# Kernel optimization log

Hardware: AMD Instinct MI355X
Metric: run time of the kernel (lower is better)

## Reference

```python
import jax, jax.numpy as jnp
import numpy as np
from jax import lax

KH = KW = 3
DIL = 4
D = DIL * (KH - 1) + 1  # dilated (effective) kernel extent = 9
PAD = 4
STRIDE = 1


def setup_inputs() -> dict:
    key = jax.random.key(0)
    k1, k2, k3, k4 = jax.random.split(key, 4)
    Cin, Cout, B, H, W = 128, 128, 16, 112, 112
    fan_in = Cin * KH * KW
    x = jax.random.normal(k1, (B, Cin, H, W), dtype=jnp.float32)
    weight = jax.random.normal(k2, (Cout, Cin, KH, KW), dtype=jnp.float32) / np.sqrt(fan_in)
    # learnable positions: offsets of each kernel point inside the dilated kernel
    P = jax.random.normal(k3, (2, Cout, Cin, KH, KW), dtype=jnp.float32) * (DIL / 2.0)
    bias = jax.random.normal(k4, (Cout,), dtype=jnp.float32) * 0.01
    return {"x": x, "weight": weight, "P": P, "bias": bias}


def _construct_kernel(weight, P):
    # Place each kernel point at its (learnable) continuous position inside the
    # D x D dilated kernel via bilinear interpolation (DCLS construction).
    O, C, kh, kw = weight.shape
    base_h = jnp.arange(kh, dtype=weight.dtype) * DIL  # regular dilated grid
    base_w = jnp.arange(kw, dtype=weight.dtype) * DIL
    p_h = jnp.clip(base_h[None, None, :, None] + P[0], 0.0, D - 1)  # (O,C,kh,kw)
    p_w = jnp.clip(base_w[None, None, None, :] + P[1], 0.0, D - 1)
    fh = jnp.floor(p_h)
    fw = jnp.floor(p_w)
    rh = p_h - fh  # fractional residuals -> bilinear weights
    rw = p_w - fw
    ih = fh.astype(jnp.int32)
    iw = fw.astype(jnp.int32)
    ih1 = jnp.minimum(ih + 1, D - 1)
    iw1 = jnp.minimum(iw + 1, D - 1)
    o = jnp.arange(O)[:, None, None, None]
    c = jnp.arange(C)[None, :, None, None]
    K = jnp.zeros((O, C, D, D), dtype=weight.dtype)
    K = K.at[o, c, ih, iw].add(weight * (1 - rh) * (1 - rw))
    K = K.at[o, c, ih1, iw].add(weight * rh * (1 - rw))
    K = K.at[o, c, ih, iw1].add(weight * (1 - rh) * rw)
    K = K.at[o, c, ih1, iw1].add(weight * rh * rw)
    return K


def reference(x, weight, P, bias):
    K = _construct_kernel(weight, P)  # (Cout, Cin, D, D)
    out = lax.conv_general_dilated(
        x, K,
        window_strides=(STRIDE, STRIDE),
        padding=[(PAD, PAD), (PAD, PAD)],
        dimension_numbers=("NCHW", "OIHW", "NCHW"),
        feature_group_count=1,
    )
    return out + bias[None, :, None, None]
```

## Files before the change

### kernel.cpp

```cpp
#include <hip/hip_runtime.h>
#include <hip/hip_bf16.h>
#include <stdint.h>


typedef __attribute__((ext_vector_type(8))) short short8;
typedef __attribute__((ext_vector_type(4))) short s16x4;
typedef __attribute__((ext_vector_type(16))) float f32x16;

__device__ inline unsigned short f2bf(float f) {
    union { float f; unsigned int u; } v; v.f = f;
    unsigned int u = v.u;
    return (unsigned short)((u + 0x7FFFu + ((u >> 16) & 1u)) >> 16);
}

__global__ void build_K(const float* __restrict__ weight,
                        const float* __restrict__ P,
                        unsigned short* __restrict__ Kws) {
    __shared__ float sacc[128 * 81];
    int tid = threadIdx.x;
    int o = blockIdx.x;
    int c = tid;
    float* a = &sacc[c * 81];
    for (int i = 0; i < 81; ++i) a[i] = 0.0f;
    int base = (o * 128 + c) * 9;
    #pragma unroll
    for (int kh = 0; kh < 3; ++kh) {
        #pragma unroll
        for (int kw = 0; kw < 3; ++kw) {
            int kk = kh * 3 + kw;
            float w  = weight[base + kk];
            float p0 = P[base + kk];
            float p1 = P[128 * 128 * 9 + base + kk];
            float ph = fminf(fmaxf((float)(kh * 4) + p0, 0.0f), 8.0f);
            float pw = fminf(fmaxf((float)(kw * 4) + p1, 0.0f), 8.0f);
            float fh = floorf(ph), fw = floorf(pw);
            float rh = ph - fh, rw = pw - fw;
            int ih = (int)fh, iw = (int)fw;
            int ih1 = min(ih + 1, 8), iw1 = min(iw + 1, 8);
            a[ih  * 9 + iw ] += w * (1.0f - rh) * (1.0f - rw);
            a[ih1 * 9 + iw ] += w * rh * (1.0f - rw);
            a[ih  * 9 + iw1] += w * (1.0f - rh) * rw;
            a[ih1 * 9 + iw1] += w * rh * rw;
        }
    }
    __syncthreads();
    for (int u = tid; u < 1296; u += 128) {
        int tap = u >> 4;
        int rem = u & 15;
        int chunk = rem >> 1, half = rem & 1;
        int c0 = chunk * 16 + half * 8;
        short8 v;
        #pragma unroll
        for (int j = 0; j < 8; ++j)
            v[j] = (short)f2bf(sacc[(c0 + j) * 81 + tap]);
        *(short8*)(Kws + ((tap * 8 + chunk) * 2 + half) * 1024 + o * 8) = v;
    }
}

__device__ __forceinline__ void dma3g(const char* Kc, char* dst, int h,
                                      int woff, int lane16) {
    const char* src = Kc + (size_t)(3 * h) * 32768 + woff + lane16;
    #pragma unroll
    for (int j = 0; j < 3; ++j)
        __builtin_amdgcn_global_load_lds(
            (const __attribute__((address_space(1))) char*)(src + (size_t)j * 32768),
            (__attribute__((address_space(3))) char*)(dst + j * 4096 + woff),
            16, 0, 0);
}

__global__ __launch_bounds__(256, 2)
void dcls_conv(const float* __restrict__ x,
               const unsigned short* __restrict__ Kws,
               const float* __restrict__ bias,
               float* __restrict__ out) {
    __shared__ __align__(16) char sX[18432];
    __shared__ __align__(16) char sK0[12288];
    __shared__ __align__(16) char sK1[12288];
    __shared__ __align__(16) char sK2[12288];

    int bid = blockIdx.x;
    int b   = bid / 49;
    int rem = bid % 49;
    int ty  = rem / 7, tx = rem % 7;
    int y0  = ty * 16, x0 = tx * 16;

    int tid  = threadIdx.x;
    int lane = tid & 63;
    int wave = tid >> 6;
    int mgrp = wave >> 1;
    int ngrp = wave & 1;
    int half = lane >> 5;
    int l31  = lane & 31;
    int lrow = (lane >> 4) & 1;
    int lcol = lane & 15;
    int woff = wave * 1024;
    int lane16 = lane * 16;

    f32x16 acc[2][4];
    #pragma unroll
    for (int i = 0; i < 2; ++i)
        #pragma unroll
        for (int j = 0; j < 4; ++j)
            #pragma unroll
            for (int k = 0; k < 16; ++k) acc[i][j][k] = 0.0f;

    int preA0 = half * 2048 + ((mgrp * 2 + 0) * 32 + l31) * 16;
    int preA1 = half * 2048 + ((mgrp * 2 + 1) * 32 + l31) * 16;
    int preB[4];
    #pragma unroll
    for (int j = 0; j < 4; ++j)
        preB[j] = (2 * (ngrp * 4 + j) + lrow) * 768 + half * 384 + lcol * 16;

    const char* __restrict__ Kb = (const char*)Kws;

    {
        #pragma unroll
        for (int it = 0; it < 5; ++it) {
            int u = tid + it * 256;
            if (u < 1152) {
                int r  = u / 48;
                int rr = u % 48;
                int hf = rr / 24;
                int co = rr % 24;
                int h = y0 - 4 + r;
                int w = x0 - 4 + co;
                bool ok = (h >= 0) & (h < 112) & (w >= 0) & (w < 112);
                const float* xp = x + ((b * 128 + hf * 8) * 12544 + h * 112 + w);
                short8 v;
                #pragma unroll
                for (int j = 0; j < 8; ++j) {
                    float f = ok ? xp[j * 12544] : 0.0f;
                    v[j] = (short)f2bf(f);
                }
                *(short8*)(sX + u * 16) = v;
            }
        }
    }
    __syncthreads();

#define KBUF(i) ((i) == 0 ? sK0 : (i) == 1 ? sK1 : sK2)

#define GRP(G) do {                                                          \
    if ((G) == 26)                                                           \
        asm volatile("s_waitcnt vmcnt(0)\n\ts_barrier" ::: "memory");        \
    else if ((G)==4||(G)==5||(G)==13||(G)==14||(G)==22||(G)==23)             \
        asm volatile("s_waitcnt vmcnt(15)\n\ts_barrier" ::: "memory");       \
    else                                                                     \
        asm volatile("s_waitcnt vmcnt(3)\n\ts_barrier" ::: "memory");        \
    if ((G) <= 24) dma3g(Kc, KBUF(((G) + 2) % 3), (G) + 2, woff, lane16);    \
    if ((G) == 3 || (G) == 12 || (G) == 21) {                                \
        const int bi_ = (G) / 9;                                             \
        _Pragma("unroll")                                                    \
        for (int i2 = 0; i2 < 3; ++i2) {                                     \
            int q_ = 3 * bi_ + i2;                                           \
            int V_ = q_ * 128 + (tid >> 1);                                  \
            int hp_ = tid & 1;                                               \
            int r_ = V_ / 48, rr_ = V_ % 48;                                 \
            int hf_ = rr_ / 24, co_ = rr_ % 24;                              \
            int h_ = y0 - 4 + r_, w_ = x0 - 4 + co_;                         \
            int hc_ = min(max(h_, 0), 111), wc_ = min(max(w_, 0), 111);      \
            okm[i2] = (h_ >= 0) & (h_ < 112) & (w_ >= 0) & (w_ < 112);       \
            const float* xp_ = x + ((b * 128 + nb + hf_ * 8 + hp_ * 4) * 12544 \
                                    + hc_ * 112 + wc_);                      \
            _Pragma("unroll")                                                \
            for (int j2 = 0; j2 < 4; ++j2)                                   \
                raw[i2 * 4 + j2] = xp_[j2 * 12544];                          \
        }                                                                    \
    }                                                                        \
    if ((G) == 6 || (G) == 15 || (G) == 24) {                                \
        const int bi_ = (G) / 9;                                             \
        _Pragma("unroll")                                                    \
        for (int i2 = 0; i2 < 3; ++i2) {                                     \
            s16x4 v_;                                                        \
            _Pragma("unroll")                                                \
            for (int j2 = 0; j2 < 4; ++j2) {                                 \
                float f_ = okm[i2] ? raw[i2 * 4 + j2] : 0.0f;                \
                v_[j2] = (short)f2bf(f_);                                    \
            }                                                                \
            stg[3 * bi_ + i2] = v_;                                          \
        }                                                                    \
    }                                                                        \
    {                                                                        \
        const char* kb_ = KBUF((G) % 3);                                     \
        _Pragma("unroll")                                                    \
        for (int j = 0; j < 3; ++j) {                                        \
            int tap_ = 3 * (G) + j;                                          \
            int tapoff_ = (tap_ / 9) * 768 + (tap_ % 9) * 16;                \
            short8 af0 = *(const short8*)(kb_ + j * 4096 + preA0);           \
            short8 af1 = *(const short8*)(kb_ + j * 4096 + preA1);           \
            short8 b0 = *(const short8*)(sX + preB[0] + tapoff_);            \
            short8 b1 = *(const short8*)(sX + preB[1] + tapoff_);            \
            short8 b2 = *(const short8*)(sX + preB[2] + tapoff_);            \
            short8 b3 = *(const short8*)(sX + preB[3] + tapoff_);            \
            acc[0][0] = __builtin_amdgcn_mfma_f32_32x32x16_bf16(af0, b0, acc[0][0], 0, 0, 0); \
            acc[1][0] = __builtin_amdgcn_mfma_f32_32x32x16_bf16(af1, b0, acc[1][0], 0, 0, 0); \
            acc[0][1] = __builtin_amdgcn_mfma_f32_32x32x16_bf16(af0, b1, acc[0][1], 0, 0, 0); \
            acc[1][1] = __builtin_amdgcn_mfma_f32_32x32x16_bf16(af1, b1, acc[1][1], 0, 0, 0); \
            acc[0][2] = __builtin_amdgcn_mfma_f32_32x32x16_bf16(af0, b2, acc[0][2], 0, 0, 0); \
            acc[1][2] = __builtin_amdgcn_mfma_f32_32x32x16_bf16(af1, b2, acc[1][2], 0, 0, 0); \
            acc[0][3] = __builtin_amdgcn_mfma_f32_32x32x16_bf16(af0, b3, acc[0][3], 0, 0, 0); \
            acc[1][3] = __builtin_amdgcn_mfma_f32_32x32x16_bf16(af1, b3, acc[1][3], 0, 0, 0); \
        }                                                                    \
    }                                                                        \
} while (0)

    for (int cc = 0; cc < 8; ++cc) {
        const char* Kc = Kb + (cc << 12);
        int nb = ((cc + 1) & 7) << 4;
        float raw[12];
        s16x4 stg[9];
        int okm[3];

        dma3g(Kc, sK0, 0, woff, lane16);
        dma3g(Kc, sK1, 1, woff, lane16);

        GRP(0);  GRP(1);  GRP(2);  GRP(3);  GRP(4);  GRP(5);  GRP(6);
        GRP(7);  GRP(8);  GRP(9);  GRP(10); GRP(11); GRP(12); GRP(13);
        GRP(14); GRP(15); GRP(16); GRP(17); GRP(18); GRP(19); GRP(20);
        GRP(21); GRP(22); GRP(23); GRP(24); GRP(25); GRP(26);

        asm volatile("s_barrier" ::: "memory");
        #pragma unroll
        for (int q = 0; q < 9; ++q)
            *(s16x4*)(sX + q * 2048 + tid * 8) = stg[q];
        __syncthreads();
    }

#undef GRP
#undef KBUF

    #pragma unroll
    for (int i = 0; i < 2; ++i) {
        int ob = (mgrp * 2 + i) * 32;
        #pragma unroll
        for (int r = 0; r < 16; ++r) {
            int o = ob + (r & 3) + 8 * (r >> 2) + 4 * half;
            float bv = bias[o];
            #pragma unroll
            for (int j = 0; j < 4; ++j) {
                int nt  = ngrp * 4 + j;
                int row = y0 + 2 * nt + lrow;
                int col = x0 + lcol;
                out[((b * 128 + o) * 112 + row) * 112 + col] = acc[i][j][r] + bv;
            }
        }
    }
}

extern "C" void kernel_launch(void* const* d_in, const int* in_sizes, int n_in,
                              void* d_out, int out_size, void* d_ws, size_t ws_size,
                              hipStream_t stream) {
    const float* x      = (const float*)d_in[0];
    const float* weight = (const float*)d_in[1];
    const float* P      = (const float*)d_in[2];
    const float* bias   = (const float*)d_in[3];
    float* out = (float*)d_out;
    unsigned short* Kws = (unsigned short*)d_ws;

    build_K<<<128, 128, 0, stream>>>(weight, P, Kws);
    dcls_conv<<<784, 256, 0, stream>>>(x, Kws, bias, out);
}
```

Before: 601.1 us.

## Load weight fragments directly to registers and double-buffer input tile in LDS

Removes the LDS staging of the weight slices through global_load_lds DMA and the per-group barriers. Each wave now loads its A fragments straight from global memory into registers, one group ahead. The input tile gets two LDS buffers, so the next channel chunk is written directly into the alternate buffer during compute instead of being held in staging registers. This drops most barriers inside the group loop but adds direct global loads (likely L2 hits) on the MFMA critical path and raises register pressure.

```diff
diff --git a/kernel.cpp b/kernel.cpp
--- a/kernel.cpp
+++ b/kernel.cpp
@@ -57,26 +57,13 @@
     }
 }
 
-__device__ __forceinline__ void dma3g(const char* Kc, char* dst, int h,
-                                      int woff, int lane16) {
-    const char* src = Kc + (size_t)(3 * h) * 32768 + woff + lane16;
-    #pragma unroll
-    for (int j = 0; j < 3; ++j)
-        __builtin_amdgcn_global_load_lds(
-            (const __attribute__((address_space(1))) char*)(src + (size_t)j * 32768),
-            (__attribute__((address_space(3))) char*)(dst + j * 4096 + woff),
-            16, 0, 0);
-}
-
 __global__ __launch_bounds__(256, 2)
 void dcls_conv(const float* __restrict__ x,
                const unsigned short* __restrict__ Kws,
                const float* __restrict__ bias,
                float* __restrict__ out) {
-    __shared__ __align__(16) char sX[18432];
-    __shared__ __align__(16) char sK0[12288];
-    __shared__ __align__(16) char sK1[12288];
-    __shared__ __align__(16) char sK2[12288];
+    __shared__ __align__(16) char sXa[18432];
+    __shared__ __align__(16) char sXb[18432];
 
     int bid = blockIdx.x;
     int b   = bid / 49;
@@ -93,8 +80,6 @@
     int l31  = lane & 31;
     int lrow = (lane >> 4) & 1;
     int lcol = lane & 15;
-    int woff = wave * 1024;
-    int lane16 = lane * 16;
 
     f32x16 acc[2][4];
     #pragma unroll
@@ -132,24 +117,26 @@
                     float f = ok ? xp[j * 12544] : 0.0f;
                     v[j] = (short)f2bf(f);
                 }
-                *(short8*)(sX + u * 16) = v;
+                *(short8*)(sXa + u * 16) = v;
             }
         }
     }
     __syncthreads();
 
-#define KBUF(i) ((i) == 0 ? sK0 : (i) == 1 ? sK1 : sK2)
+#define LOADA(G, P) do {                                                     \
+    const char* kp_ = KA + (size_t)(3 * (G)) * 32768;                        \
+    afr[P][0] = *(const short8*)(kp_ + preA0);                               \
+    afr[P][1] = *(const short8*)(kp_ + preA1);                               \
+    afr[P][2] = *(const short8*)(kp_ + 32768 + preA0);                       \
+    afr[P][3] = *(const short8*)(kp_ + 32768 + preA1);                       \
+    afr[P][4] = *(const short8*)(kp_ + 65536 + preA0);                       \
+    afr[P][5] = *(const short8*)(kp_ + 65536 + preA1);                       \
+} while (0)
 
 #define GRP(G) do {                                                          \
-    if ((G) == 26)                                                           \
-        asm volatile("s_waitcnt vmcnt(0)\n\ts_barrier" ::: "memory");        \
-    else if ((G)==4||(G)==5||(G)==13||(G)==14||(G)==22||(G)==23)             \
-        asm volatile("s_waitcnt vmcnt(15)\n\ts_barrier" ::: "memory");       \
-    else                                                                     \
-        asm volatile("s_waitcnt vmcnt(3)\n\ts_barrier" ::: "memory");        \
-    if ((G) <= 24) dma3g(Kc, KBUF(((G) + 2) % 3), (G) + 2, woff, lane16);    \
-    if ((G) == 3 || (G) == 12 || (G) == 21) {                                \
-        const int bi_ = (G) / 9;                                             \
+    if ((G) < 26) LOADA((G) + 1, ((G) + 1) & 1);                             \
+    if (((G) == 6 || (G) == 12 || (G) == 18) && cc < 7) {                    \
+        const int bi_ = ((G) - 6) / 6;                                       \
         _Pragma("unroll")                                                    \
         for (int i2 = 0; i2 < 3; ++i2) {                                     \
             int q_ = 3 * bi_ + i2;                                           \
@@ -167,67 +154,63 @@
                 raw[i2 * 4 + j2] = xp_[j2 * 12544];                          \
         }                                                                    \
     }                                                                        \
-    if ((G) == 6 || (G) == 15 || (G) == 24) {                                \
-        const int bi_ = (G) / 9;                                             \
+    if (((G) == 9 || (G) == 15 || (G) == 21) && cc < 7) {                    \
+        const int bi_ = ((G) - 9) / 6;                                       \
         _Pragma("unroll")                                                    \
         for (int i2 = 0; i2 < 3; ++i2) {                                     \
+            int q_ = 3 * bi_ + i2;                                           \
             s16x4 v_;                                                        \
             _Pragma("unroll")                                                \
             for (int j2 = 0; j2 < 4; ++j2) {                                 \
                 float f_ = okm[i2] ? raw[i2 * 4 + j2] : 0.0f;                \
                 v_[j2] = (short)f2bf(f_);                                    \
             }                                                                \
-            stg[3 * bi_ + i2] = v_;                                          \
+            *(s16x4*)(sXw + q_ * 2048 + tid * 8) = v_;                       \
         }                                                                    \
     }                                                                        \
     {                                                                        \
-        const char* kb_ = KBUF((G) % 3);                                     \
+        const int p_ = (G) & 1;                                              \
         _Pragma("unroll")                                                    \
         for (int j = 0; j < 3; ++j) {                                        \
             int tap_ = 3 * (G) + j;                                          \
             int tapoff_ = (tap_ / 9) * 768 + (tap_ % 9) * 16;                \
-            short8 af0 = *(const short8*)(kb_ + j * 4096 + preA0);           \
-            short8 af1 = *(const short8*)(kb_ + j * 4096 + preA1);           \
-            short8 b0 = *(const short8*)(sX + preB[0] + tapoff_);            \
-            short8 b1 = *(const short8*)(sX + preB[1] + tapoff_);            \
-            short8 b2 = *(const short8*)(sX + preB[2] + tapoff_);            \
-            short8 b3 = *(const short8*)(sX + preB[3] + tapoff_);            \
-            acc[0][0] = __builtin_amdgcn_mfma_f32_32x32x16_bf16(af0, b0, acc[0][0], 0, 0, 0); \
-            acc[1][0] = __builtin_amdgcn_mfma_f32_32x32x16_bf16(af1, b0, acc[1][0], 0, 0, 0); \
-            acc[0][1] = __builtin_amdgcn_mfma_f32_32x32x16_bf16(af0, b1, acc[0][1], 0, 0, 0); \
-            acc[1][1] = __builtin_amdgcn_mfma_f32_32x32x16_bf16(af1, b1, acc[1][1], 0, 0, 0); \
-            acc[0][2] = __builtin_amdgcn_mfma_f32_32x32x16_bf16(af0, b2, acc[0][2], 0, 0, 0); \
-            acc[1][2] = __builtin_amdgcn_mfma_f32_32x32x16_bf16(af1, b2, acc[1][2], 0, 0, 0); \
-            acc[0][3] = __builtin_amdgcn_mfma_f32_32x32x16_bf16(af0, b3, acc[0][3], 0, 0, 0); \
-            acc[1][3] = __builtin_amdgcn_mfma_f32_32x32x16_bf16(af1, b3, acc[1][3], 0, 0, 0); \
+            short8 b0 = *(const short8*)(sXr + preB[0] + tapoff_);           \
+            short8 b1 = *(const short8*)(sXr + preB[1] + tapoff_);           \
+            short8 b2 = *(const short8*)(sXr + preB[2] + tapoff_);           \
+            short8 b3 = *(const short8*)(sXr + preB[3] + tapoff_);           \
+            acc[0][0] = __builtin_amdgcn_mfma_f32_32x32x16_bf16(afr[p_][j*2+0], b0, acc[0][0], 0, 0, 0); \
+            acc[1][0] = __builtin_amdgcn_mfma_f32_32x32x16_bf16(afr[p_][j*2+1], b0, acc[1][0], 0, 0, 0); \
+            acc[0][1] = __builtin_amdgcn_mfma_f32_32x32x16_bf16(afr[p_][j*2+0], b1, acc[0][1], 0, 0, 0); \
+            acc[1][1] = __builtin_amdgcn_mfma_f32_32x32x16_bf16(afr[p_][j*2+1], b1, acc[1][1], 0, 0, 0); \
+            acc[0][2] = __builtin_amdgcn_mfma_f32_32x32x16_bf16(afr[p_][j*2+0], b2, acc[0][2], 0, 0, 0); \
+            acc[1][2] = __builtin_amdgcn_mfma_f32_32x32x16_bf16(afr[p_][j*2+1], b2, acc[1][2], 0, 0, 0); \
+            acc[0][3] = __builtin_amdgcn_mfma_f32_32x32x16_bf16(afr[p_][j*2+0], b3, acc[0][3], 0, 0, 0); \
+            acc[1][3] = __builtin_amdgcn_mfma_f32_32x32x16_bf16(afr[p_][j*2+1], b3, acc[1][3], 0, 0, 0); \
         }                                                                    \
     }                                                                        \
 } while (0)
 
     for (int cc = 0; cc < 8; ++cc) {
-        const char* Kc = Kb + (cc << 12);
+        const char* KA = Kb + (cc << 12);
+        const char* sXr = (cc & 1) ? sXb : sXa;
+        char*       sXw = (cc & 1) ? sXa : sXb;
         int nb = ((cc + 1) & 7) << 4;
         float raw[12];
-        s16x4 stg[9];
         int okm[3];
 
-        dma3g(Kc, sK0, 0, woff, lane16);
-        dma3g(Kc, sK1, 1, woff, lane16);
+        short8 afr[2][6];
+        LOADA(0, 0);
 
         GRP(0);  GRP(1);  GRP(2);  GRP(3);  GRP(4);  GRP(5);  GRP(6);
         GRP(7);  GRP(8);  GRP(9);  GRP(10); GRP(11); GRP(12); GRP(13);
         GRP(14); GRP(15); GRP(16); GRP(17); GRP(18); GRP(19); GRP(20);
         GRP(21); GRP(22); GRP(23); GRP(24); GRP(25); GRP(26);
 
-        asm volatile("s_barrier" ::: "memory");
-        #pragma unroll
-        for (int q = 0; q < 9; ++q)
-            *(s16x4*)(sX + q * 2048 + tid * 8) = stg[q];
         __syncthreads();
     }
 
 #undef GRP
-#undef KBUF
+#undef LOADA
 
     #pragma unroll
     for (int i = 0; i < 2; ++i) {
```

Measured after the change: 653.3 us. 1.09x slower.
